# Kernel tuning notes

Measured on AMD Instinct MI355X. Metric: run time of the kernel, lower is better.

The kernel has to match this reference:

```python
import jax, jax.numpy as jnp
import numpy as np
from functools import partial

N = 512
H, W = 324, 332
C = 120
NEAR, FAR, BG = 0.01, 100.0, 1.0


def setup_inputs() -> dict:
    key = jax.random.key(0)
    k1, k2, k3, k4, k5, k6 = jax.random.split(key, 6)
    # positions: small xy, depth z in [2, 8] so everything projects on screen
    xy = 0.5 * jax.random.normal(k1, (N, 2), dtype=jnp.float32)
    z = jax.random.uniform(k2, (N, 1), dtype=jnp.float32, minval=2.0, maxval=8.0)
    positions = jnp.concatenate([xy, z], axis=-1)  # [N,3]
    rotations = jax.random.normal(k3, (N, 4), dtype=jnp.float32)  # unused by the math
    # scales in [0.5, 4.5] pixels -> small footprints, early-break never triggers
    scales = jax.random.uniform(k4, (N, 3), dtype=jnp.float32) * 4.0 + 0.5
    opacities = jax.random.uniform(k5, (N,), dtype=jnp.float32)
    spectral_features = jax.random.uniform(k6, (N, C), dtype=jnp.float32)
    tone_mapping = jnp.ones((C,), dtype=jnp.float32)
    intrinsics = jnp.array([[300.0, 0.0, 166.0],
                            [0.0, 300.0, 162.0],
                            [0.0, 0.0, 1.0]], dtype=jnp.float32)
    extrinsics = jnp.eye(4, dtype=jnp.float32)
    return {"positions": positions, "rotations": rotations, "scales": scales,
            "opacities": opacities, "spectral_features": spectral_features,
            "tone_mapping": tone_mapping, "intrinsics": intrinsics,
            "extrinsics": extrinsics}


def _render(positions, scales, opacities, spectral_features, tone_mapping,
            intrinsics, extrinsics):
    # --- projection (world -> camera -> screen) ---
    ph = jnp.concatenate([positions, jnp.ones_like(positions[:, :1])], axis=-1)  # [N,4]
    cam = ph @ extrinsics.T                     # [N,4]
    cam3 = cam[:, :3]
    proj = cam3 @ intrinsics.T                  # [N,3]
    screen = proj[:, :2] / (proj[:, 2:3] + 1e-6)  # [N,2] (x, y)
    depths = cam3[:, 2]                         # [N]

    # --- frustum / screen culling mask (kept as a validity flag) ---
    valid = (depths > NEAR) & (depths < FAR)
    valid &= (screen[:, 0] > -100.0) & (screen[:, 0] < W + 100.0)
    valid &= (screen[:, 1] > -100.0) & (screen[:, 1] < H + 100.0)

    # --- 2D covariance: diag(scale_x^2, scale_y^2), regularized inverse ---
    s2 = scales[:, :2] ** 2
    cov = jnp.zeros((positions.shape[0], 2, 2), dtype=positions.dtype)
    cov = cov.at[:, 0, 0].set(s2[:, 0]).at[:, 1, 1].set(s2[:, 1])
    cov_inv = jnp.linalg.inv(cov + 1e-4 * jnp.eye(2, dtype=positions.dtype))  # [N,2,2]

    # --- depth sort (front to back) ---
    order = jnp.argsort(depths)
    screen_s = screen[order]
    depths_s = depths[order]
    cinv_s = cov_inv[order]
    op_s = opacities[order]
    valid_s = valid[order]
    spec_s = spectral_features[order]           # [N,C]

    # pixel grid: pix[h,w] = (x=w, y=h)
    X, Y = jnp.meshgrid(jnp.arange(W), jnp.arange(H))  # each [H,W]
    pix = jnp.stack([X, Y], axis=-1).astype(positions.dtype)  # [H,W,2]

    def step(A, g):
        pos, cinv, op, v = g
        done = jnp.mean(A) > 0.99  # torch early-break condition
        off = (pos[0] < -W) | (pos[0] > 2 * W) | (pos[1] < -H) | (pos[1] > 2 * H)
        skip = done | off | jnp.logical_not(v)
        diff = pix - pos                                    # [H,W,2]
        mahal = jnp.einsum('hwi,ij,hwj->hw', diff, cinv, diff)
        alpha = op * jnp.exp(-0.5 * mahal) * (1.0 - A)      # [H,W]
        alpha = jnp.where(skip, 0.0, alpha)
        return A + alpha, alpha

    A0 = jnp.zeros((H, W), dtype=positions.dtype)
    A_final, alphas = jax.lax.scan(step, A0, (screen_s, cinv_s, op_s, valid_s))  # alphas [N,H,W]

    # spectral/depth accumulation == sum_i feature_i * alpha_i (GEMM over N)
    spectral = jnp.einsum('nc,nhw->chw', spec_s, alphas)    # [C,H,W]
    depth_img = jnp.einsum('n,nhw->hw', depths_s, alphas)   # [H,W]
    spectral = spectral + BG * (1.0 - A_final)[None]
    spectral = spectral * tone_mapping[:, None, None]
    return spectral, depth_img, A_final


def reference(positions, rotations, scales, opacities, spectral_features,
              tone_mapping, intrinsics, extrinsics):
    # rotations are accepted but unused by the original math (diagonal 2D cov)
    return _render(positions, scales, opacities, spectral_features,
                   tone_mapping, intrinsics, extrinsics)
```

## Files before the change

kernel.cpp:

```cpp
#include <hip/hip_runtime.h>
#include <math.h>

#define N_G 512
#define IMG_H 324
#define IMG_W 332
#define N_C 120
#define HW (IMG_H*IMG_W)
#define CHUNK 64
#define TSX 21
#define TSY 81
#define NT (TSX*TSY)
#define NBLK 512


#define ACC4(i) \
  { float4 s4 = *(const float4*)(row + 4*(i)); \
    a##i.x = fmaf(wv, s4.x, a##i.x); \
    a##i.y = fmaf(wv, s4.y, a##i.y); \
    a##i.z = fmaf(wv, s4.z, a##i.z); \
    a##i.w = fmaf(wv, s4.w, a##i.w); }

#define WR4(i) \
  { slot[4*(i)+0]=a##i.x; slot[4*(i)+1]=a##i.y; \
    slot[4*(i)+2]=a##i.z; slot[4*(i)+3]=a##i.w; }

#define CMB4(i) \
  { float4 t4 = *(const float4*)(tmh + 4*(i)); \
    out[(cbase + 4*(i) + 0)*HW + pixi] = (a##i.x + slot[4*(i)+0] + bgT)*t4.x; \
    out[(cbase + 4*(i) + 1)*HW + pixi] = (a##i.y + slot[4*(i)+1] + bgT)*t4.y; \
    out[(cbase + 4*(i) + 2)*HW + pixi] = (a##i.z + slot[4*(i)+2] + bgT)*t4.z; \
    out[(cbase + 4*(i) + 3)*HW + pixi] = (a##i.w + slot[4*(i)+3] + bgT)*t4.w; }

__global__ __launch_bounds__(256, 2) void k_render(
    const float* __restrict__ pos, const float* __restrict__ scales,
    const float* __restrict__ opac, const float* __restrict__ Km,
    const float* __restrict__ Em, const float* __restrict__ spec,
    const float* __restrict__ tm, float* __restrict__ out)
{
  __shared__ float prm[N_G*8];
  __shared__ float buf[CHUNK*64];
  __shared__ float sbuf[CHUNK*N_C];
  __shared__ float Tcar[64], Dcar[64];
  __shared__ int wcnt[4];

  const int tid  = threadIdx.x;
  const int w    = tid >> 6;
  const int lane = tid & 63;
  const int h    = w & 1;
  const int s    = w >> 1;
  const int tx = lane & 15, ty = lane >> 4;
  const int cbase = h*60;
  const unsigned long long ltm = (1ull << lane) - 1ull;

  float psx[2], psy[2], pc00[2], pc11[2], pl2[2], pd[2];
  float bxmin[2], bxmax[2], bymin[2], bymax[2];
  {
    const float E0=Em[0],E1=Em[1],E2=Em[2],E3=Em[3],
                E4=Em[4],E5=Em[5],E6=Em[6],E7=Em[7],
                E8=Em[8],E9=Em[9],E10=Em[10],E11=Em[11];
    const float K0=Km[0],K1=Km[1],K2=Km[2],
                K3=Km[3],K4=Km[4],K5=Km[5],
                K6=Km[6],K7=Km[7],K8=Km[8];
    #pragma unroll
    for (int q = 0; q < 2; ++q) {
      const int g = w*128 + lane + q*64;
      float p0 = pos[g*3+0], p1 = pos[g*3+1], p2 = pos[g*3+2];
      float cam0 = E0*p0 + E1*p1 + E2*p2  + E3;
      float cam1 = E4*p0 + E5*p1 + E6*p2  + E7;
      float cam2 = E8*p0 + E9*p1 + E10*p2 + E11;
      float pr0 = K0*cam0 + K1*cam1 + K2*cam2;
      float pr1 = K3*cam0 + K4*cam1 + K5*cam2;
      float pr2 = K6*cam0 + K7*cam1 + K8*cam2;
      float inv = 1.0f/(pr2 + 1e-6f);
      float sx = pr0*inv, sy = pr1*inv;
      float depth = cam2;
      bool valid = (depth > 0.01f) && (depth < 100.0f)
                && (sx > -100.0f) && (sx < (float)IMG_W + 100.0f)
                && (sy > -100.0f) && (sy < (float)IMG_H + 100.0f);
      bool off = (sx < -(float)IMG_W) || (sx > 2.0f*(float)IMG_W)
              || (sy < -(float)IMG_H) || (sy > 2.0f*(float)IMG_H);
      bool skip = off || (!valid);
      float s0 = scales[g*3+0], s1 = scales[g*3+1];
      float v0 = s0*s0 + 1e-4f, v1 = s1*s1 + 1e-4f;
      const float HL2E = 0.72134752f;
      psx[q] = sx; psy[q] = sy;
      pc00[q] = HL2E/v0; pc11[q] = HL2E/v1;
      pl2[q] = __log2f(skip ? 0.0f : opac[g]);
      pd[q]  = depth;
      float rx = 6.0f*sqrtf(v0);
      float ry = 6.0f*sqrtf(v1);
      bxmin[q] = skip ?  1e9f : sx - rx;
      bxmax[q] = skip ? -1e9f : sx + rx;
      bymin[q] = skip ?  1e9f : sy - ry;
      bymax[q] = skip ? -1e9f : sy + ry;
    }
  }

  for (int t = blockIdx.x; t < NT; t += NBLK) {
    const int jx = t % TSX, ky = t / TSX;
    const int bx = 10 + ((jx & 1) ? ((jx+1)>>1) : -((jx+1)>>1));
    const int by = 40 + ((ky & 1) ? ((ky+1)>>1) : -((ky+1)>>1));

    const int x = bx*16 + tx;
    const int y = by*4 + ty;
    const bool inb = (x < IMG_W) && (y < IMG_H);
    const float px = (float)min(x, IMG_W-1);
    const float py = (float)min(y, IMG_H-1);
    const float wxmin = (float)(bx*16), wxmax = wxmin + 15.0f;
    const float wymin = (float)(by*4),  wymax = wymin + 3.0f;

    bool h0 = !(bxmin[0] > wxmax || bxmax[0] < wxmin ||
                bymin[0] > wymax || bymax[0] < wymin);
    bool h1 = !(bxmin[1] > wxmax || bxmax[1] < wxmin ||
                bymin[1] > wymax || bymax[1] < wymin);
    unsigned long long m0 = __ballot(h0), m1 = __ballot(h1);
    int c0 = __popcll(m0);
    if (lane == 0) wcnt[w] = c0 + __popcll(m1);
    __syncthreads();
    int offw = 0;
    #pragma unroll
    for (int k = 0; k < 4; ++k) if (k < w) offw += wcnt[k];
    const int nh = wcnt[0] + wcnt[1] + wcnt[2] + wcnt[3];
    const int p0 = offw + __popcll(m0 & ltm);
    const int p1 = offw + c0 + __popcll(m1 & ltm);
    if (h0) buf[p0] = pd[0];
    if (h1) buf[p1] = pd[1];
    if (tid < 4) buf[nh + tid] = 1e30f;
    __syncthreads();

    if (h0 | h1) {
      int r0 = 0, r1 = 0;
      const float d0 = pd[0], d1 = pd[1];
      for (int j = 0; j < nh; j += 4) {
        float4 k4 = *(const float4*)&buf[j];
        if (h0) {
          r0 += (k4.x < d0 || (k4.x == d0 && j+0 < p0)) ? 1 : 0;
          r0 += (k4.y < d0 || (k4.y == d0 && j+1 < p0)) ? 1 : 0;
          r0 += (k4.z < d0 || (k4.z == d0 && j+2 < p0)) ? 1 : 0;
          r0 += (k4.w < d0 || (k4.w == d0 && j+3 < p0)) ? 1 : 0;
        }
        if (h1) {
          r1 += (k4.x < d1 || (k4.x == d1 && j+0 < p1)) ? 1 : 0;
          r1 += (k4.y < d1 || (k4.y == d1 && j+1 < p1)) ? 1 : 0;
          r1 += (k4.z < d1 || (k4.z == d1 && j+2 < p1)) ? 1 : 0;
          r1 += (k4.w < d1 || (k4.w == d1 && j+3 < p1)) ? 1 : 0;
        }
      }
      if (h0) {
        *(float4*)&prm[r0*8]   = make_float4(psx[0], psy[0], pc00[0], pc11[0]);
        *(float4*)&prm[r0*8+4] = make_float4(pl2[0], pd[0],
                                   __int_as_float((w*128 + lane)*N_C), 0.0f);
      }
      if (h1) {
        *(float4*)&prm[r1*8]   = make_float4(psx[1], psy[1], pc00[1], pc11[1]);
        *(float4*)&prm[r1*8+4] = make_float4(pl2[1], pd[1],
                                   __int_as_float((w*128 + lane + 64)*N_C), 0.0f);
      }
    }
    __syncthreads();

    float T = 1.0f, dacc = 0.0f;
    float4 a0={0,0,0,0}, a1={0,0,0,0}, a2={0,0,0,0}, a3={0,0,0,0}, a4={0,0,0,0},
           a5={0,0,0,0}, a6={0,0,0,0}, a7={0,0,0,0}, a8={0,0,0,0}, a9={0,0,0,0},
           a10={0,0,0,0}, a11={0,0,0,0}, a12={0,0,0,0}, a13={0,0,0,0}, a14={0,0,0,0};

    for (int cb = 0; cb < nh; cb += CHUNK) {
      const int nc = min(CHUNK, nh - cb);

      #pragma unroll 2
      for (int j = w; j < nc; j += 4) {
        float4 q0 = *(const float4*)&prm[(cb+j)*8];
        float4 q1 = *(const float4*)&prm[(cb+j)*8+4];
        float dx = px - q0.x, dy = py - q0.y;
        float m = q0.z*dx*dx + q0.w*dy*dy;
        buf[j*64 + lane] = exp2f(q1.x - m);
        int sbase = __float_as_int(q1.z);
        sbuf[j*N_C + lane] = spec[sbase + lane];
        if (lane < N_C - 64) sbuf[j*N_C + 64 + lane] = spec[sbase + 64 + lane];
      }
      __syncthreads();

      if (w == 0) {
        #pragma unroll 4
        for (int j = 0; j < nc; ++j) {
          float a = buf[j*64 + lane];
          float wv = a * T;
          buf[j*64 + lane] = wv;
          T -= wv;
          dacc = fmaf(prm[(cb+j)*8+5], wv, dacc);
        }
      }
      __syncthreads();

      #pragma unroll 2
      for (int j = s; j < nc; j += 2) {
        float wv = buf[j*64 + lane];
        const float* row = &sbuf[j*N_C + cbase];
        ACC4(0)  ACC4(1)  ACC4(2)  ACC4(3)  ACC4(4)
        ACC4(5)  ACC4(6)  ACC4(7)  ACC4(8)  ACC4(9)
        ACC4(10) ACC4(11) ACC4(12) ACC4(13) ACC4(14)
      }
      __syncthreads();
    }

    if (w == 0) { Tcar[lane] = T; Dcar[lane] = dacc; }
    if (s == 1) {
      float* slot = (h == 0 ? buf : sbuf) + lane*61;
      WR4(0)  WR4(1)  WR4(2)  WR4(3)  WR4(4)
      WR4(5)  WR4(6)  WR4(7)  WR4(8)  WR4(9)
      WR4(10) WR4(11) WR4(12) WR4(13) WR4(14)
    }
    __syncthreads();

    if (s == 0 && inb) {
      const int pixi = y*IMG_W + x;
      const float Tf = Tcar[lane];
      const float bgT = Tf;
      const float* tmh = tm + cbase;
      const float* slot = (h == 0 ? buf : sbuf) + lane*61;
      CMB4(0)  CMB4(1)  CMB4(2)  CMB4(3)  CMB4(4)
      CMB4(5)  CMB4(6)  CMB4(7)  CMB4(8)  CMB4(9)
      CMB4(10) CMB4(11) CMB4(12) CMB4(13) CMB4(14)
      if (h == 0) out[N_C*HW + pixi] = Dcar[lane];
      else        out[N_C*HW + HW + pixi] = 1.0f - Tf;
    }
    __syncthreads();
  }
}

extern "C" void kernel_launch(void* const* d_in, const int* in_sizes, int n_in,
                              void* d_out, int out_size, void* d_ws, size_t ws_size,
                              hipStream_t stream) {
  const float* pos    = (const float*)d_in[0];
  const float* scales = (const float*)d_in[2];
  const float* opac   = (const float*)d_in[3];
  const float* spec   = (const float*)d_in[4];
  const float* tm     = (const float*)d_in[5];
  const float* K      = (const float*)d_in[6];
  const float* E      = (const float*)d_in[7];
  float* out = (float*)d_out;
  (void)d_ws; (void)ws_size;

  k_render<<<NBLK, 256, 0, stream>>>(pos, scales, opac, K, E, spec, tm, out);
}
```

Baseline: 124.0 us.

## Launch one block per tile and split channels across all four waves

Replaces the persistent grid-stride loop with one block per 16x4 tile (NT blocks). The spectral accumulation now splits the 120 channels over all four waves in interleaved float4 groups, instead of splitting over two channel halves and two gaussian halves. That removes the cross-wave partial-sum write and combine through shared memory. It also lowers CHUNK to 48 and raises the launch-bounds occupancy hint to 3 blocks per CU, and switches the transmittance update to T *= (1-a). The cost is that every block recomputes projection and culling for all 512 gaussians, and the image is covered by many more blocks.

```diff
diff --git a/kernel.cpp b/kernel.cpp
--- a/kernel.cpp
+++ b/kernel.cpp
@@ -6,32 +6,13 @@
 #define IMG_W 332
 #define N_C 120
 #define HW (IMG_H*IMG_W)
-#define CHUNK 64
+#define CHUNK 48
 #define TSX 21
 #define TSY 81
 #define NT (TSX*TSY)
-#define NBLK 512
-
-
-#define ACC4(i) \
-  { float4 s4 = *(const float4*)(row + 4*(i)); \
-    a##i.x = fmaf(wv, s4.x, a##i.x); \
-    a##i.y = fmaf(wv, s4.y, a##i.y); \
-    a##i.z = fmaf(wv, s4.z, a##i.z); \
-    a##i.w = fmaf(wv, s4.w, a##i.w); }
-
-#define WR4(i) \
-  { slot[4*(i)+0]=a##i.x; slot[4*(i)+1]=a##i.y; \
-    slot[4*(i)+2]=a##i.z; slot[4*(i)+3]=a##i.w; }
-
-#define CMB4(i) \
-  { float4 t4 = *(const float4*)(tmh + 4*(i)); \
-    out[(cbase + 4*(i) + 0)*HW + pixi] = (a##i.x + slot[4*(i)+0] + bgT)*t4.x; \
-    out[(cbase + 4*(i) + 1)*HW + pixi] = (a##i.y + slot[4*(i)+1] + bgT)*t4.y; \
-    out[(cbase + 4*(i) + 2)*HW + pixi] = (a##i.z + slot[4*(i)+2] + bgT)*t4.z; \
-    out[(cbase + 4*(i) + 3)*HW + pixi] = (a##i.w + slot[4*(i)+3] + bgT)*t4.w; }
-
-__global__ __launch_bounds__(256, 2) void k_render(
+
+
+__global__ __launch_bounds__(256, 3) void k_render(
     const float* __restrict__ pos, const float* __restrict__ scales,
     const float* __restrict__ opac, const float* __restrict__ Km,
     const float* __restrict__ Em, const float* __restrict__ spec,
@@ -46,10 +27,7 @@
   const int tid  = threadIdx.x;
   const int w    = tid >> 6;
   const int lane = tid & 63;
-  const int h    = w & 1;
-  const int s    = w >> 1;
   const int tx = lane & 15, ty = lane >> 4;
-  const int cbase = h*60;
   const unsigned long long ltm = (1ull << lane) - 1ull;
 
   float psx[2], psy[2], pc00[2], pc11[2], pl2[2], pd[2];
@@ -96,135 +74,138 @@
     }
   }
 
-  for (int t = blockIdx.x; t < NT; t += NBLK) {
-    const int jx = t % TSX, ky = t / TSX;
-    const int bx = 10 + ((jx & 1) ? ((jx+1)>>1) : -((jx+1)>>1));
-    const int by = 40 + ((ky & 1) ? ((ky+1)>>1) : -((ky+1)>>1));
-
-    const int x = bx*16 + tx;
-    const int y = by*4 + ty;
-    const bool inb = (x < IMG_W) && (y < IMG_H);
-    const float px = (float)min(x, IMG_W-1);
-    const float py = (float)min(y, IMG_H-1);
-    const float wxmin = (float)(bx*16), wxmax = wxmin + 15.0f;
-    const float wymin = (float)(by*4),  wymax = wymin + 3.0f;
-
-    bool h0 = !(bxmin[0] > wxmax || bxmax[0] < wxmin ||
-                bymin[0] > wymax || bymax[0] < wymin);
-    bool h1 = !(bxmin[1] > wxmax || bxmax[1] < wxmin ||
-                bymin[1] > wymax || bymax[1] < wymin);
-    unsigned long long m0 = __ballot(h0), m1 = __ballot(h1);
-    int c0 = __popcll(m0);
-    if (lane == 0) wcnt[w] = c0 + __popcll(m1);
+  const int t = blockIdx.x;
+  const int jx = t % TSX, ky = t / TSX;
+  const int bx = 10 + ((jx & 1) ? ((jx+1)>>1) : -((jx+1)>>1));
+  const int by = 40 + ((ky & 1) ? ((ky+1)>>1) : -((ky+1)>>1));
+
+  const int x = bx*16 + tx;
+  const int y = by*4 + ty;
+  const bool inb = (x < IMG_W) && (y < IMG_H);
+  const float px = (float)min(x, IMG_W-1);
+  const float py = (float)min(y, IMG_H-1);
+  const float wxmin = (float)(bx*16), wxmax = wxmin + 15.0f;
+  const float wymin = (float)(by*4),  wymax = wymin + 3.0f;
+
+  bool h0 = !(bxmin[0] > wxmax || bxmax[0] < wxmin ||
+              bymin[0] > wymax || bymax[0] < wymin);
+  bool h1 = !(bxmin[1] > wxmax || bxmax[1] < wxmin ||
+              bymin[1] > wymax || bymax[1] < wymin);
+  unsigned long long m0 = __ballot(h0), m1 = __ballot(h1);
+  int c0 = __popcll(m0);
+  if (lane == 0) wcnt[w] = c0 + __popcll(m1);
+  __syncthreads();
+  int offw = 0;
+  #pragma unroll
+  for (int k = 0; k < 4; ++k) if (k < w) offw += wcnt[k];
+  const int nh = wcnt[0] + wcnt[1] + wcnt[2] + wcnt[3];
+  const int p0 = offw + __popcll(m0 & ltm);
+  const int p1 = offw + c0 + __popcll(m1 & ltm);
+  if (h0) buf[p0] = pd[0];
+  if (h1) buf[p1] = pd[1];
+  if (tid < 4) buf[nh + tid] = 1e30f;
+  __syncthreads();
+
+  if (h0 | h1) {
+    int r0 = 0, r1 = 0;
+    const float d0 = pd[0], d1 = pd[1];
+    for (int j = 0; j < nh; j += 4) {
+      float4 k4 = *(const float4*)&buf[j];
+      if (h0) {
+        r0 += (k4.x < d0 || (k4.x == d0 && j+0 < p0)) ? 1 : 0;
+        r0 += (k4.y < d0 || (k4.y == d0 && j+1 < p0)) ? 1 : 0;
+        r0 += (k4.z < d0 || (k4.z == d0 && j+2 < p0)) ? 1 : 0;
+        r0 += (k4.w < d0 || (k4.w == d0 && j+3 < p0)) ? 1 : 0;
+      }
+      if (h1) {
+        r1 += (k4.x < d1 || (k4.x == d1 && j+0 < p1)) ? 1 : 0;
+        r1 += (k4.y < d1 || (k4.y == d1 && j+1 < p1)) ? 1 : 0;
+        r1 += (k4.z < d1 || (k4.z == d1 && j+2 < p1)) ? 1 : 0;
+        r1 += (k4.w < d1 || (k4.w == d1 && j+3 < p1)) ? 1 : 0;
+      }
+    }
+    if (h0) {
+      *(float4*)&prm[r0*8]   = make_float4(psx[0], psy[0], pc00[0], pc11[0]);
+      *(float4*)&prm[r0*8+4] = make_float4(pl2[0], pd[0],
+                                 __int_as_float((w*128 + lane)*N_C), 0.0f);
+    }
+    if (h1) {
+      *(float4*)&prm[r1*8]   = make_float4(psx[1], psy[1], pc00[1], pc11[1]);
+      *(float4*)&prm[r1*8+4] = make_float4(pl2[1], pd[1],
+                                 __int_as_float((w*128 + lane + 64)*N_C), 0.0f);
+    }
+  }
+  __syncthreads();
+
+  float T = 1.0f, dacc = 0.0f;
+  float4 acc[8] = {};
+
+  for (int cb = 0; cb < nh; cb += CHUNK) {
+    const int nc = min(CHUNK, nh - cb);
+
+    #pragma unroll 2
+    for (int j = w; j < nc; j += 4) {
+      float4 q0 = *(const float4*)&prm[(cb+j)*8];
+      float4 q1 = *(const float4*)&prm[(cb+j)*8+4];
+      float dx = px - q0.x, dy = py - q0.y;
+      float m = q0.z*dx*dx + q0.w*dy*dy;
+      buf[j*64 + lane] = exp2f(q1.x - m);
+      int sbase = __float_as_int(q1.z);
+      sbuf[j*N_C + lane] = spec[sbase + lane];
+      if (lane < N_C - 64) sbuf[j*N_C + 64 + lane] = spec[sbase + 64 + lane];
+    }
     __syncthreads();
-    int offw = 0;
+
+    if (w == 0) {
+      #pragma unroll 4
+      for (int j = 0; j < nc; ++j) {
+        float a  = buf[j*64 + lane];
+        float wv = a * T;
+        buf[j*64 + lane] = wv;
+        dacc = fmaf(prm[(cb+j)*8+5], wv, dacc);
+        T *= (1.0f - a);
+      }
+    }
+    __syncthreads();
+
+    #pragma unroll 2
+    for (int j = 0; j < nc; ++j) {
+      float wv = buf[j*64 + lane];
+      const float* base = &sbuf[j*N_C];
+      #pragma unroll
+      for (int gi = 0; gi < 8; ++gi) {
+        const int g = w + 4*gi;
+        if (g < 30) {
+          float4 s4 = *(const float4*)(base + 4*g);
+          acc[gi].x = fmaf(wv, s4.x, acc[gi].x);
+          acc[gi].y = fmaf(wv, s4.y, acc[gi].y);
+          acc[gi].z = fmaf(wv, s4.z, acc[gi].z);
+          acc[gi].w = fmaf(wv, s4.w, acc[gi].w);
+        }
+      }
+    }
+    __syncthreads();
+  }
+
+  if (w == 0) { Tcar[lane] = T; Dcar[lane] = dacc; }
+  __syncthreads();
+
+  if (inb) {
+    const int pixi = y*IMG_W + x;
+    const float bgT = Tcar[lane];
     #pragma unroll
-    for (int k = 0; k < 4; ++k) if (k < w) offw += wcnt[k];
-    const int nh = wcnt[0] + wcnt[1] + wcnt[2] + wcnt[3];
-    const int p0 = offw + __popcll(m0 & ltm);
-    const int p1 = offw + c0 + __popcll(m1 & ltm);
-    if (h0) buf[p0] = pd[0];
-    if (h1) buf[p1] = pd[1];
-    if (tid < 4) buf[nh + tid] = 1e30f;
-    __syncthreads();
-
-    if (h0 | h1) {
-      int r0 = 0, r1 = 0;
-      const float d0 = pd[0], d1 = pd[1];
-      for (int j = 0; j < nh; j += 4) {
-        float4 k4 = *(const float4*)&buf[j];
-        if (h0) {
-          r0 += (k4.x < d0 || (k4.x == d0 && j+0 < p0)) ? 1 : 0;
-          r0 += (k4.y < d0 || (k4.y == d0 && j+1 < p0)) ? 1 : 0;
-          r0 += (k4.z < d0 || (k4.z == d0 && j+2 < p0)) ? 1 : 0;
-          r0 += (k4.w < d0 || (k4.w == d0 && j+3 < p0)) ? 1 : 0;
-        }
-        if (h1) {
-          r1 += (k4.x < d1 || (k4.x == d1 && j+0 < p1)) ? 1 : 0;
-          r1 += (k4.y < d1 || (k4.y == d1 && j+1 < p1)) ? 1 : 0;
-          r1 += (k4.z < d1 || (k4.z == d1 && j+2 < p1)) ? 1 : 0;
-          r1 += (k4.w < d1 || (k4.w == d1 && j+3 < p1)) ? 1 : 0;
-        }
-      }
-      if (h0) {
-        *(float4*)&prm[r0*8]   = make_float4(psx[0], psy[0], pc00[0], pc11[0]);
-        *(float4*)&prm[r0*8+4] = make_float4(pl2[0], pd[0],
-                                   __int_as_float((w*128 + lane)*N_C), 0.0f);
-      }
-      if (h1) {
-        *(float4*)&prm[r1*8]   = make_float4(psx[1], psy[1], pc00[1], pc11[1]);
-        *(float4*)&prm[r1*8+4] = make_float4(pl2[1], pd[1],
-                                   __int_as_float((w*128 + lane + 64)*N_C), 0.0f);
-      }
-    }
-    __syncthreads();
-
-    float T = 1.0f, dacc = 0.0f;
-    float4 a0={0,0,0,0}, a1={0,0,0,0}, a2={0,0,0,0}, a3={0,0,0,0}, a4={0,0,0,0},
-           a5={0,0,0,0}, a6={0,0,0,0}, a7={0,0,0,0}, a8={0,0,0,0}, a9={0,0,0,0},
-           a10={0,0,0,0}, a11={0,0,0,0}, a12={0,0,0,0}, a13={0,0,0,0}, a14={0,0,0,0};
-
-    for (int cb = 0; cb < nh; cb += CHUNK) {
-      const int nc = min(CHUNK, nh - cb);
-
-      #pragma unroll 2
-      for (int j = w; j < nc; j += 4) {
-        float4 q0 = *(const float4*)&prm[(cb+j)*8];
-        float4 q1 = *(const float4*)&prm[(cb+j)*8+4];
-        float dx = px - q0.x, dy = py - q0.y;
-        float m = q0.z*dx*dx + q0.w*dy*dy;
-        buf[j*64 + lane] = exp2f(q1.x - m);
-        int sbase = __float_as_int(q1.z);
-        sbuf[j*N_C + lane] = spec[sbase + lane];
-        if (lane < N_C - 64) sbuf[j*N_C + 64 + lane] = spec[sbase + 64 + lane];
-      }
-      __syncthreads();
-
-      if (w == 0) {
-        #pragma unroll 4
-        for (int j = 0; j < nc; ++j) {
-          float a = buf[j*64 + lane];
-          float wv = a * T;
-          buf[j*64 + lane] = wv;
-          T -= wv;
-          dacc = fmaf(prm[(cb+j)*8+5], wv, dacc);
-        }
-      }
-      __syncthreads();
-
-      #pragma unroll 2
-      for (int j = s; j < nc; j += 2) {
-        float wv = buf[j*64 + lane];
-        const float* row = &sbuf[j*N_C + cbase];
-        ACC4(0)  ACC4(1)  ACC4(2)  ACC4(3)  ACC4(4)
-        ACC4(5)  ACC4(6)  ACC4(7)  ACC4(8)  ACC4(9)
-        ACC4(10) ACC4(11) ACC4(12) ACC4(13) ACC4(14)
-      }
-      __syncthreads();
-    }
-
-    if (w == 0) { Tcar[lane] = T; Dcar[lane] = dacc; }
-    if (s == 1) {
-      float* slot = (h == 0 ? buf : sbuf) + lane*61;
-      WR4(0)  WR4(1)  WR4(2)  WR4(3)  WR4(4)
-      WR4(5)  WR4(6)  WR4(7)  WR4(8)  WR4(9)
-      WR4(10) WR4(11) WR4(12) WR4(13) WR4(14)
-    }
-    __syncthreads();
-
-    if (s == 0 && inb) {
-      const int pixi = y*IMG_W + x;
-      const float Tf = Tcar[lane];
-      const float bgT = Tf;
-      const float* tmh = tm + cbase;
-      const float* slot = (h == 0 ? buf : sbuf) + lane*61;
-      CMB4(0)  CMB4(1)  CMB4(2)  CMB4(3)  CMB4(4)
-      CMB4(5)  CMB4(6)  CMB4(7)  CMB4(8)  CMB4(9)
-      CMB4(10) CMB4(11) CMB4(12) CMB4(13) CMB4(14)
-      if (h == 0) out[N_C*HW + pixi] = Dcar[lane];
-      else        out[N_C*HW + HW + pixi] = 1.0f - Tf;
-    }
-    __syncthreads();
+    for (int gi = 0; gi < 8; ++gi) {
+      const int g = w + 4*gi;
+      if (g < 30) {
+        float4 t4 = *(const float4*)&tm[4*g];
+        out[(4*g+0)*HW + pixi] = (acc[gi].x + bgT)*t4.x;
+        out[(4*g+1)*HW + pixi] = (acc[gi].y + bgT)*t4.y;
+        out[(4*g+2)*HW + pixi] = (acc[gi].z + bgT)*t4.z;
+        out[(4*g+3)*HW + pixi] = (acc[gi].w + bgT)*t4.w;
+      }
+    }
+    if (w == 0) out[N_C*HW + pixi] = Dcar[lane];
+    if (w == 1) out[N_C*HW + HW + pixi] = 1.0f - Tcar[lane];
   }
 }
 
@@ -241,5 +222,5 @@
   float* out = (float*)d_out;
   (void)d_ws; (void)ws_size;
 
-  k_render<<<NBLK, 256, 0, stream>>>(pos, scales, opac, K, E, spec, tm, out);
+  k_render<<<NT, 256, 0, stream>>>(pos, scales, opac, K, E, spec, tm, out);
 }
```

Measured after the change: 129.3 us. 4.4% more time.
